# Optimization experiments

Hardware: AMD Instinct MI355X
Metric: run time of the kernel (lower is better)

The kernel has to match this reference:

```python
import jax
import jax.numpy as jnp
import numpy as np

N = 256   # hardcoded in the torch module via expand(256, 256)
D = 256
K = 16
M_MARGIN = 0.6
T_THRESH = 0.0025
EPS = 1e-12


def setup_inputs() -> dict:
    key = jax.random.key(0)
    k1, k2 = jax.random.split(key)
    yi = jax.random.normal(k1, (N, D), dtype=jnp.float32)
    yi_t = jax.random.normal(k2, (N, D), dtype=jnp.float32)
    return {"yi": yi, "yi_t": yi_t}


def _l2_normalize(x):
    return x / jnp.sqrt(jnp.sum(x * x, axis=-1, keepdims=True) + EPS)


def reference(yi, yi_t):
    yi_n = _l2_normalize(yi)      # [N, D]
    yit_n = _l2_normalize(yi_t)   # [N, D]

    # pairwise half-distances: [N, N]
    diff = yi_n[:, None, :] - yi_n[None, :, :]           # [N, N, D]
    dis_yii = 0.5 * jnp.sqrt(jnp.sum(diff * diff, axis=-1) + EPS)

    # K+1 smallest distances per row (self is smallest)
    neg_vals, topk_idx = jax.lax.top_k(-dis_yii, K + 1)  # [N, K+1]
    nbr_idx = topk_idx[:, 1:]                            # [N, K] exclude self

    yj = yi_n[nbr_idx]                                   # [N, K, D]
    dis_yij = 0.5 * jnp.sqrt(jnp.sum((yi_n[:, None, :] - yj) ** 2, axis=-1) + EPS)
    dis_yi_tj = 0.5 * jnp.sqrt(jnp.sum((yit_n[:, None, :] - yj) ** 2, axis=-1) + EPS)

    e1 = jnp.sum((dis_yij - dis_yi_tj) ** 2 - T_THRESH)

    # margin term: dist(yi, yi_t) + m - (second smallest pairwise dist)
    dis_yi_yi_t = 0.5 * jnp.sqrt(jnp.sum((yi_n - yit_n) ** 2, axis=-1) + EPS)  # [N]
    second_nn = -neg_vals[:, 1]                          # [N]
    out = dis_yi_yi_t + M_MARGIN - second_nn
    e2 = jnp.sum(jnp.maximum(out, 0.0))

    return e1 + e2
```

## Files before the change

### kernel.cpp

```cpp
#include <hip/hip_runtime.h>
#include <math.h>

#define NN 256
#define DD 256
#define KK 16
#define M_MARGIN 0.6f
#define T_THRESH 0.0025f
#define EPS 1e-12f

__global__ void __launch_bounds__(256) normalize_kernel(
    const float* __restrict__ yi, const float* __restrict__ yit,
    float* __restrict__ yin, float* __restrict__ yitn,
    float* __restrict__ out)
{
    const int row  = blockIdx.x & (NN - 1);
    const bool a   = blockIdx.x < NN;
    const float* src = a ? yi  : yit;
    float*       dst = a ? yin : yitn;
    const int t = threadIdx.x;

    float v = src[row * DD + t];
    float s = v * v;
    #pragma unroll
    for (int off = 32; off > 0; off >>= 1) s += __shfl_down(s, off, 64);

    __shared__ float ws[4];
    if ((t & 63) == 0) ws[t >> 6] = s;
    __syncthreads();
    float total = ws[0] + ws[1] + ws[2] + ws[3];

    dst[row * DD + t] = v / sqrtf(total + EPS);

    if (blockIdx.x == 0 && t == 0) out[0] = 0.0f;
}

__global__ void __launch_bounds__(256) blcd_main_kernel(
    const float* __restrict__ yin, const float* __restrict__ yitn,
    float* __restrict__ out)
{
    __shared__ float s_yi[DD];
    __shared__ float s_yit[DD];
    __shared__ float sdis[NN];
    __shared__ float sdist[NN];
    __shared__ float lds4[4];
    __shared__ float s_disiit;

    const int i = blockIdx.x;
    const int t = threadIdx.x;

    s_yi[t]  = yin [i * DD + t];
    s_yit[t] = yitn[i * DD + t];
    __syncthreads();

    {
        float df = s_yi[t] - s_yit[t];
        float v  = df * df;
        #pragma unroll
        for (int off = 32; off > 0; off >>= 1) v += __shfl_down(v, off, 64);
        if ((t & 63) == 0) lds4[t >> 6] = v;
        __syncthreads();
        if (t == 0)
            s_disiit = 0.5f * sqrtf(lds4[0] + lds4[1] + lds4[2] + lds4[3] + EPS);
    }

    const float* rowj = yin + t * DD;
    float d2 = 0.0f, dt2 = 0.0f;
    #pragma unroll 8
    for (int d = 0; d < DD; ++d) {
        float b = rowj[d];
        float u = s_yi[d]  - b;
        float w = s_yit[d] - b;
        d2  += u * u;
        dt2 += w * w;
    }
    sdis[t]  = 0.5f * sqrtf(d2  + EPS);
    sdist[t] = 0.5f * sqrtf(dt2 + EPS);
    __syncthreads();

    const float myv = sdis[t];
    int rank = 0;
    for (int j = 0; j < NN; ++j) {
        float vj = sdis[j];
        rank += (vj < myv || (vj == myv && j < t)) ? 1 : 0;
    }

    float contrib = 0.0f;
    if (rank >= 1 && rank <= KK) {
        float dd = myv - sdist[t];
        contrib = dd * dd - T_THRESH;
    }
    if (rank == 1) {
        float o = s_disiit + M_MARGIN - myv;
        contrib += fmaxf(o, 0.0f);
    }

    #pragma unroll
    for (int off = 32; off > 0; off >>= 1) contrib += __shfl_down(contrib, off, 64);
    __syncthreads();
    if ((t & 63) == 0) lds4[t >> 6] = contrib;
    __syncthreads();
    if (t == 0) atomicAdd(out, lds4[0] + lds4[1] + lds4[2] + lds4[3]);
}

extern "C" void kernel_launch(void* const* d_in, const int* in_sizes, int n_in,
                              void* d_out, int out_size, void* d_ws, size_t ws_size,
                              hipStream_t stream) {
    (void)in_sizes; (void)n_in; (void)out_size; (void)ws_size;

    const float* yi  = (const float*)d_in[0];
    const float* yit = (const float*)d_in[1];
    float* out = (float*)d_out;

    float* yin  = (float*)d_ws;
    float* yitn = (float*)d_ws + NN * DD;

    normalize_kernel<<<2 * NN, 256, 0, stream>>>(yi, yit, yin, yitn, out);
    blcd_main_kernel<<<NN, 256, 0, stream>>>(yin, yitn, out);
}
```

Before: 76.37 us.

## Fuse normalization into main kernel using dot-product distance identity

Removes the separate normalize kernel and the workspace round-trip. Each block computes raw norms and cross dots with warp reductions, and each thread computes dot products of its row against the staged raw rows, then converts them to distances via sqrt(2-2cos). The row loads and the LDS rank scan are vectorized to float4. The output is zeroed with hipMemsetAsync, and the cancellation-prone cosine form may shift near-tie orderings in top-k.

```diff
diff --git a/kernel.cpp b/kernel.cpp
--- a/kernel.cpp
+++ b/kernel.cpp
@@ -8,112 +8,107 @@
 #define T_THRESH 0.0025f
 #define EPS 1e-12f
 
-__global__ void __launch_bounds__(256) normalize_kernel(
+__global__ void __launch_bounds__(256) blcd_fused_kernel(
     const float* __restrict__ yi, const float* __restrict__ yit,
-    float* __restrict__ yin, float* __restrict__ yitn,
-    float* __restrict__ out)
-{
-    const int row  = blockIdx.x & (NN - 1);
-    const bool a   = blockIdx.x < NN;
-    const float* src = a ? yi  : yit;
-    float*       dst = a ? yin : yitn;
-    const int t = threadIdx.x;
-
-    float v = src[row * DD + t];
-    float s = v * v;
-    #pragma unroll
-    for (int off = 32; off > 0; off >>= 1) s += __shfl_down(s, off, 64);
-
-    __shared__ float ws[4];
-    if ((t & 63) == 0) ws[t >> 6] = s;
-    __syncthreads();
-    float total = ws[0] + ws[1] + ws[2] + ws[3];
-
-    dst[row * DD + t] = v / sqrtf(total + EPS);
-
-    if (blockIdx.x == 0 && t == 0) out[0] = 0.0f;
-}
-
-__global__ void __launch_bounds__(256) blcd_main_kernel(
-    const float* __restrict__ yin, const float* __restrict__ yitn,
     float* __restrict__ out)
 {
     __shared__ float s_yi[DD];
     __shared__ float s_yit[DD];
     __shared__ float sdis[NN];
-    __shared__ float sdist[NN];
-    __shared__ float lds4[4];
-    __shared__ float s_disiit;
+    __shared__ float red[12];
 
     const int i = blockIdx.x;
     const int t = threadIdx.x;
 
-    s_yi[t]  = yin [i * DD + t];
-    s_yit[t] = yitn[i * DD + t];
+    const float a = yi [i * DD + t];
+    const float b = yit[i * DD + t];
+    s_yi[t]  = a;
+    s_yit[t] = b;
+
+    float r0 = a * a, r1 = b * b, r2 = a * b;
+    #pragma unroll
+    for (int off = 32; off > 0; off >>= 1) {
+        r0 += __shfl_down(r0, off, 64);
+        r1 += __shfl_down(r1, off, 64);
+        r2 += __shfl_down(r2, off, 64);
+    }
+    const int w = t >> 6;
+    if ((t & 63) == 0) { red[w] = r0; red[4 + w] = r1; red[8 + w] = r2; }
     __syncthreads();
 
-    {
-        float df = s_yi[t] - s_yit[t];
-        float v  = df * df;
-        #pragma unroll
-        for (int off = 32; off > 0; off >>= 1) v += __shfl_down(v, off, 64);
-        if ((t & 63) == 0) lds4[t >> 6] = v;
-        __syncthreads();
-        if (t == 0)
-            s_disiit = 0.5f * sqrtf(lds4[0] + lds4[1] + lds4[2] + lds4[3] + EPS);
+    const float nn_i  = red[0] + red[1] + red[2]  + red[3];
+    const float nn_it = red[4] + red[5] + red[6]  + red[7];
+    const float cross = red[8] + red[9] + red[10] + red[11];
+    const float inv_ni  = 1.0f / sqrtf(nn_i  + EPS);
+    const float inv_nit = 1.0f / sqrtf(nn_it + EPS);
+
+    const float4* __restrict__ rj  = (const float4*)(yi + t * DD);
+    const float4* __restrict__ si  = (const float4*)s_yi;
+    const float4* __restrict__ sit = (const float4*)s_yit;
+    float4 q4  = make_float4(0.f, 0.f, 0.f, 0.f);
+    float4 qt4 = make_float4(0.f, 0.f, 0.f, 0.f);
+    float4 nn4 = make_float4(0.f, 0.f, 0.f, 0.f);
+    #pragma unroll 8
+    for (int d = 0; d < DD / 4; ++d) {
+        float4 y = rj[d];
+        float4 u = si[d];
+        float4 v = sit[d];
+        q4.x  += y.x * u.x; q4.y  += y.y * u.y; q4.z  += y.z * u.z; q4.w  += y.w * u.w;
+        qt4.x += y.x * v.x; qt4.y += y.y * v.y; qt4.z += y.z * v.z; qt4.w += y.w * v.w;
+        nn4.x += y.x * y.x; nn4.y += y.y * y.y; nn4.z += y.z * y.z; nn4.w += y.w * y.w;
     }
+    const float q  = (q4.x  + q4.y ) + (q4.z  + q4.w );
+    const float qt = (qt4.x + qt4.y) + (qt4.z + qt4.w);
+    const float nn = (nn4.x + nn4.y) + (nn4.z + nn4.w);
 
-    const float* rowj = yin + t * DD;
-    float d2 = 0.0f, dt2 = 0.0f;
-    #pragma unroll 8
-    for (int d = 0; d < DD; ++d) {
-        float b = rowj[d];
-        float u = s_yi[d]  - b;
-        float w = s_yit[d] - b;
-        d2  += u * u;
-        dt2 += w * w;
-    }
-    sdis[t]  = 0.5f * sqrtf(d2  + EPS);
-    sdist[t] = 0.5f * sqrtf(dt2 + EPS);
+    const float inv_nt = 1.0f / sqrtf(nn + EPS);
+    const float c    = q  * inv_nt * inv_ni;
+    const float ct   = qt * inv_nt * inv_nit;
+    const float myv  = 0.5f * sqrtf(fmaxf(2.0f - 2.0f * c , 0.0f) + EPS);
+    const float myvt = 0.5f * sqrtf(fmaxf(2.0f - 2.0f * ct, 0.0f) + EPS);
+    sdis[t] = myv;
     __syncthreads();
 
-    const float myv = sdis[t];
     int rank = 0;
-    for (int j = 0; j < NN; ++j) {
-        float vj = sdis[j];
-        rank += (vj < myv || (vj == myv && j < t)) ? 1 : 0;
+    const float4* sd4 = (const float4*)sdis;
+    #pragma unroll 8
+    for (int j4 = 0; j4 < NN / 4; ++j4) {
+        float4 v = sd4[j4];
+        const int j = j4 * 4;
+        rank += (v.x < myv || (v.x == myv && (j + 0) < t)) ? 1 : 0;
+        rank += (v.y < myv || (v.y == myv && (j + 1) < t)) ? 1 : 0;
+        rank += (v.z < myv || (v.z == myv && (j + 2) < t)) ? 1 : 0;
+        rank += (v.w < myv || (v.w == myv && (j + 3) < t)) ? 1 : 0;
     }
 
     float contrib = 0.0f;
     if (rank >= 1 && rank <= KK) {
-        float dd = myv - sdist[t];
+        const float dd = myv - myvt;
         contrib = dd * dd - T_THRESH;
     }
     if (rank == 1) {
-        float o = s_disiit + M_MARGIN - myv;
-        contrib += fmaxf(o, 0.0f);
+        const float cc = cross * inv_ni * inv_nit;
+        const float d_iit = 0.5f * sqrtf(fmaxf(2.0f - 2.0f * cc, 0.0f) + EPS);
+        contrib += fmaxf(d_iit + M_MARGIN - myv, 0.0f);
     }
 
     #pragma unroll
     for (int off = 32; off > 0; off >>= 1) contrib += __shfl_down(contrib, off, 64);
     __syncthreads();
-    if ((t & 63) == 0) lds4[t >> 6] = contrib;
+    if ((t & 63) == 0) red[w] = contrib;
     __syncthreads();
-    if (t == 0) atomicAdd(out, lds4[0] + lds4[1] + lds4[2] + lds4[3]);
+    if (t == 0) atomicAdd(out, (red[0] + red[1]) + (red[2] + red[3]));
 }
 
 extern "C" void kernel_launch(void* const* d_in, const int* in_sizes, int n_in,
                               void* d_out, int out_size, void* d_ws, size_t ws_size,
                               hipStream_t stream) {
-    (void)in_sizes; (void)n_in; (void)out_size; (void)ws_size;
+    (void)in_sizes; (void)n_in; (void)out_size; (void)d_ws; (void)ws_size;
 
     const float* yi  = (const float*)d_in[0];
     const float* yit = (const float*)d_in[1];
     float* out = (float*)d_out;
 
-    float* yin  = (float*)d_ws;
-    float* yitn = (float*)d_ws + NN * DD;
-
-    normalize_kernel<<<2 * NN, 256, 0, stream>>>(yi, yit, yin, yitn, out);
-    blcd_main_kernel<<<NN, 256, 0, stream>>>(yin, yitn, out);
+    hipMemsetAsync(out, 0, sizeof(float), stream);
+    blcd_fused_kernel<<<NN, 256, 0, stream>>>(yi, yit, out);
 }
```

Measured after the change: 74.77 us. 2.1% less time.
